# Performance work log

Hardware: AMD Instinct MI355X
Metric: run time of the kernel (lower is better)

Reference implementation:

```python
import jax, jax.numpy as jnp
import numpy as np

EPS = 1e-8
NEG_INF = -9e15  # matches torch masked_fill value


def setup_inputs() -> dict:
    key = jax.random.key(0)
    k1, k2 = jax.random.split(key)
    B, D = 4096, 512
    p1 = jax.random.normal(k1, (B, D), dtype=jnp.float32)
    p2 = jax.random.normal(k2, (B, D), dtype=jnp.float32)
    return {"p1": p1, "p2": p2}


def reference(p1, p2):
    # NT-Xent / InfoNCE loss as in SimCLR_MODEL.contrastive_loss (temperature = 1).
    z = jnp.concatenate([p1, p2], axis=0)              # [N, D], N = 2B
    # cosine similarity == GEMM of L2-normalized rows (torch eps clamp = 1e-8)
    zn = z / jnp.maximum(jnp.linalg.norm(z, axis=-1, keepdims=True), EPS)
    sim = zn @ zn.T                                     # [N, N]
    N = sim.shape[0]
    idx = jnp.arange(N)
    sim = sim.at[idx, idx].set(NEG_INF)                 # mask self-similarity
    # positive pair of row i is row (i + N/2) mod N (eye rolled by N/2)
    pos = sim[idx, (idx + N // 2) % N]                  # [N]
    nll = -pos + jax.nn.logsumexp(sim, axis=-1)
    return jnp.mean(nll)
```

## Files before the change

kernel.cpp:

```cpp
#include <hip/hip_runtime.h>
#include <hip/hip_bf16.h>
#include <math.h>

#define N_TOT 8192
#define HALF_N 4096
#define D_DIM 512
#define BM 256
#define BK 64
#define NKIT (D_DIM / BK)
#define NTILES 528
#define THREADS 512

#define WAIT_VM8 0xF78
#define WAIT_VM4 0xF74
#define WAIT_VM0 0xF70

typedef float f32x4_t __attribute__((ext_vector_type(4)));
typedef long long i64x2 __attribute__((ext_vector_type(2)));

typedef __attribute__((address_space(1))) unsigned int g_u32;
typedef __attribute__((address_space(3))) unsigned int l_u32;

__global__ __launch_bounds__(256) void k_normalize(
    const float* __restrict__ p1, const float* __restrict__ p2,
    unsigned char* __restrict__ zf8, float* __restrict__ rowsum,
    float* __restrict__ out)
{
    const int w = threadIdx.x >> 6;
    const int lane = threadIdx.x & 63;
    const int row = blockIdx.x * 4 + w;

    if (threadIdx.x < 4) rowsum[blockIdx.x * 4 + threadIdx.x] = 0.0f;
    if (blockIdx.x == 0 && threadIdx.x == 0) out[0] = 0.0f;

    const float* src = (row < HALF_N) ? p1 + (size_t)row * D_DIM
                                      : p2 + (size_t)(row - HALF_N) * D_DIM;
    float4 a = *(const float4*)(src + lane * 4);
    float4 b = *(const float4*)(src + 256 + lane * 4);
    float s = a.x*a.x + a.y*a.y + a.z*a.z + a.w*a.w
            + b.x*b.x + b.y*b.y + b.z*b.z + b.w*b.w;
    #pragma unroll
    for (int m = 1; m < 64; m <<= 1) s += __shfl_xor(s, m, 64);
    float inv = 1.0f / fmaxf(sqrtf(s), 1e-8f);

    int pk0 = __builtin_amdgcn_cvt_pk_fp8_f32(a.x * inv, a.y * inv, 0, false);
    pk0     = __builtin_amdgcn_cvt_pk_fp8_f32(a.z * inv, a.w * inv, pk0, true);
    int pk1 = __builtin_amdgcn_cvt_pk_fp8_f32(b.x * inv, b.y * inv, 0, false);
    pk1     = __builtin_amdgcn_cvt_pk_fp8_f32(b.z * inv, b.w * inv, pk1, true);

    unsigned char* dst = zf8 + (size_t)row * D_DIM;
    const int o0 = lane * 4;
    const int o1 = 256 + lane * 4;
    const int d0 = (o0 & ~63) + ((o0 >> 3) & 3) * 16 + ((o0 >> 5) & 1) * 8 + (o0 & 4);
    const int d1 = (o1 & ~63) + ((o1 >> 3) & 3) * 16 + ((o1 >> 5) & 1) * 8 + (o1 & 4);
    *(int*)(dst + d0) = pk0;
    *(int*)(dst + d1) = pk1;
}

__global__ __launch_bounds__(THREADS, 2) void k_gemm(
    const unsigned char* __restrict__ zf8,
    float* __restrict__ rowsum, float* __restrict__ pos)
{
    __shared__ __align__(16) unsigned char As[4][BM * BK];
    __shared__ __align__(16) unsigned char Bs[4][BM * BK];

    const int tid = threadIdx.x;
    const int lane = tid & 63;
    const int w = tid >> 6;
    const int wr = w >> 2, wc = w & 3;
    const int q = lane >> 4, l15 = lane & 15;

    const int t0 = blockIdx.x;
    const int t = (t0 & 7) * (NTILES / 8) + (t0 >> 3);

    int bi = (int)((sqrtf(8.0f * (float)t + 1.0f) - 1.0f) * 0.5f);
    while ((bi + 1) * (bi + 2) / 2 <= t) ++bi;
    while (bi * (bi + 1) / 2 > t) --bi;
    const int bx = bi;
    const int by = t - bi * (bi + 1) / 2;
    const bool isDiag = (bx == by);
    const bool hasPos = (bx - by == (HALF_N / BM));
    const int rowBase = by * BM;
    const int colBase = bx * BM;

    const int ci0 = tid;
    const int ci1 = tid + THREADS;
    const int r0 = ci0 >> 2, cc0 = ci0 & 3;
    const int r1 = ci1 >> 2, cc1 = ci1 & 3;
    const int gc0 = cc0 ^ ((r0 >> 1) & 3);
    const int gc1 = cc1 ^ ((r1 >> 1) & 3);

    const unsigned char* gA0 = zf8 + (size_t)(rowBase + r0) * D_DIM + gc0 * 16;
    const unsigned char* gA1 = zf8 + (size_t)(rowBase + r1) * D_DIM + gc1 * 16;
    const unsigned char* gB0 = zf8 + (size_t)(colBase + r0) * D_DIM + gc0 * 16;
    const unsigned char* gB1 = zf8 + (size_t)(colBase + r1) * D_DIM + gc1 * 16;

    auto stageAll = [&](int buf, int kblk) {
        const int kb = kblk * BK;
        __builtin_amdgcn_global_load_lds((const g_u32*)(gA0 + kb), (l_u32*)&As[buf][ci0 * 16], 16, 0, 0);
        __builtin_amdgcn_global_load_lds((const g_u32*)(gA1 + kb), (l_u32*)&As[buf][ci1 * 16], 16, 0, 0);
        __builtin_amdgcn_global_load_lds((const g_u32*)(gB0 + kb), (l_u32*)&Bs[buf][ci0 * 16], 16, 0, 0);
        __builtin_amdgcn_global_load_lds((const g_u32*)(gB1 + kb), (l_u32*)&Bs[buf][ci1 * 16], 16, 0, 0);
    };

    f32x4_t acc[8][4] = {};

#define READ_A(i) do { const int ra_ = wr * 128 + (i) * 16 + l15; \
        aF[i] = *(const i64x2*)&As[cur][ra_ * BK + (q ^ ((ra_ >> 1) & 3)) * 16]; } while (0)
#define READ_B(j) do { const int rb_ = wc * 64 + (j) * 16 + l15; \
        bF[j] = *(const i64x2*)&Bs[cur][rb_ * BK + (q ^ ((rb_ >> 1) & 3)) * 16]; } while (0)
#define QUAD(ih, jh) do { \
        __builtin_amdgcn_s_setprio(1); \
        _Pragma("unroll") for (int h_ = 0; h_ < 2; h_++) \
        _Pragma("unroll") for (int i_ = 0; i_ < 4; i_++) \
        _Pragma("unroll") for (int j_ = 0; j_ < 2; j_++) \
            acc[(ih) * 4 + i_][(jh) * 2 + j_] = __builtin_amdgcn_mfma_f32_16x16x32_fp8_fp8( \
                aF[(ih) * 4 + i_][h_], bF[(jh) * 2 + j_][h_], acc[(ih) * 4 + i_][(jh) * 2 + j_], 0, 0, 0); \
        __builtin_amdgcn_s_setprio(0); } while (0)

    stageAll(0, 0);
    stageAll(1, 1);
    stageAll(2, 2);
    __builtin_amdgcn_s_waitcnt(WAIT_VM8);
    __builtin_amdgcn_s_barrier();
    __builtin_amdgcn_sched_barrier(0);

    #pragma unroll
    for (int it = 0; it < NKIT; it++) {
        const int cur = it & 3;
        const int nslot = (it + 3) & 3;
        const bool doStage = (it + 3) < NKIT;
        const int kb = (it + 3) * BK;

        i64x2 aF[8], bF[4];

        READ_A(0); READ_A(1); READ_A(2); READ_A(3);
        READ_B(0); READ_B(1);
        if (doStage)
            __builtin_amdgcn_global_load_lds((const g_u32*)(gA0 + kb), (l_u32*)&As[nslot][ci0 * 16], 16, 0, 0);
        __builtin_amdgcn_s_barrier();
        QUAD(0, 0);
        __builtin_amdgcn_s_barrier();

        READ_B(2); READ_B(3);
        if (doStage)
            __builtin_amdgcn_global_load_lds((const g_u32*)(gA1 + kb), (l_u32*)&As[nslot][ci1 * 16], 16, 0, 0);
        __builtin_amdgcn_s_barrier();
        QUAD(0, 1);
        __builtin_amdgcn_s_barrier();

        READ_A(4); READ_A(5); READ_A(6); READ_A(7);
        if (doStage)
            __builtin_amdgcn_global_load_lds((const g_u32*)(gB0 + kb), (l_u32*)&Bs[nslot][ci0 * 16], 16, 0, 0);
        __builtin_amdgcn_s_barrier();
        QUAD(1, 0);
        __builtin_amdgcn_s_barrier();

        if (doStage)
            __builtin_amdgcn_global_load_lds((const g_u32*)(gB1 + kb), (l_u32*)&Bs[nslot][ci1 * 16], 16, 0, 0);
        __builtin_amdgcn_s_barrier();
        QUAD(1, 1);
        if (it < NKIT - 1) {
            if (it < 5)       __builtin_amdgcn_s_waitcnt(WAIT_VM8);
            else if (it == 5) __builtin_amdgcn_s_waitcnt(WAIT_VM4);
            else              __builtin_amdgcn_s_waitcnt(WAIT_VM0);
            __builtin_amdgcn_s_barrier();
            __builtin_amdgcn_sched_barrier(0);
        }
    }
#undef READ_A
#undef READ_B
#undef QUAD

    float colacc[4] = {0.f, 0.f, 0.f, 0.f};
    #pragma unroll
    for (int i = 0; i < 8; i++) {
        #pragma unroll
        for (int r = 0; r < 4; r++) {
            const int row = rowBase + wr * 128 + i * 16 + q * 4 + r;
            float rs = 0.0f;
            #pragma unroll
            for (int j = 0; j < 4; j++) {
                const int col = colBase + wc * 64 + j * 16 + l15;
                const float c = acc[i][j][r];
                float e = __expf(c);
                if (isDiag && col == row) e = 0.0f;
                rs += e;
                colacc[j] += e;
                if (hasPos && col == row + HALF_N) { pos[row] = c; pos[col] = c; }
            }
            rs += __shfl_xor(rs, 1); rs += __shfl_xor(rs, 2);
            rs += __shfl_xor(rs, 4); rs += __shfl_xor(rs, 8);
            if (l15 == 0) atomicAdd(&rowsum[row], rs);
        }
    }
    if (!isDiag) {
        #pragma unroll
        for (int j = 0; j < 4; j++) {
            float cs = colacc[j];
            cs += __shfl_xor(cs, 16);
            cs += __shfl_xor(cs, 32);
            if (q == 0) atomicAdd(&rowsum[colBase + wc * 64 + j * 16 + l15], cs);
        }
    }
}

__global__ __launch_bounds__(256) void k_finalize(
    const float* __restrict__ rowsum, const float* __restrict__ pos,
    float* __restrict__ out)
{
    const int t = threadIdx.x;
    const int i = blockIdx.x * 256 + t;
    float s = logf(rowsum[i]) - pos[i];
    #pragma unroll
    for (int m = 1; m < 64; m <<= 1) s += __shfl_xor(s, m, 64);
    __shared__ float red[4];
    if ((t & 63) == 0) red[t >> 6] = s;
    __syncthreads();
    if (t == 0)
        atomicAdd(out, (red[0] + red[1] + red[2] + red[3]) * (1.0f / (float)N_TOT));
}

extern "C" void kernel_launch(void* const* d_in, const int* in_sizes, int n_in,
                              void* d_out, int out_size, void* d_ws, size_t ws_size,
                              hipStream_t stream) {
    const float* p1 = (const float*)d_in[0];
    const float* p2 = (const float*)d_in[1];

    unsigned char* zf8 = (unsigned char*)d_ws;
    float* rowsum = (float*)((char*)d_ws + (size_t)N_TOT * D_DIM);
    float* pos    = rowsum + N_TOT;
    float* outp   = (float*)d_out;

    k_normalize<<<N_TOT / 4, 256, 0, stream>>>(p1, p2, zf8, rowsum, outp);
    k_gemm<<<NTILES, THREADS, 0, stream>>>(zf8, rowsum, pos);
    k_finalize<<<N_TOT / 256, 256, 0, stream>>>(rowsum, pos, outp);
}
```

Baseline: 123.3 us.

## Reduce GEMM LDS pipeline from four stages to double buffering

Shrinks the shared-memory staging for A and B tiles from four slots to two, prefetching only one K block ahead and waiting for all loads at each iteration end. This halves LDS use per block, which should let two blocks reside per CU and improve occupancy and tail balance across the 528 tiles. In exchange, the prefetch distance drops, so global-load latency is less hidden within a block. Scheduling barriers are also added after each staging barrier.

```diff
diff --git a/kernel.cpp b/kernel.cpp
--- a/kernel.cpp
+++ b/kernel.cpp
@@ -11,8 +11,6 @@
 #define NTILES 528
 #define THREADS 512
 
-#define WAIT_VM8 0xF78
-#define WAIT_VM4 0xF74
 #define WAIT_VM0 0xF70
 
 typedef float f32x4_t __attribute__((ext_vector_type(4)));
@@ -61,8 +59,8 @@
     const unsigned char* __restrict__ zf8,
     float* __restrict__ rowsum, float* __restrict__ pos)
 {
-    __shared__ __align__(16) unsigned char As[4][BM * BK];
-    __shared__ __align__(16) unsigned char Bs[4][BM * BK];
+    __shared__ __align__(16) unsigned char As[2][BM * BK];
+    __shared__ __align__(16) unsigned char Bs[2][BM * BK];
 
     const int tid = threadIdx.x;
     const int lane = tid & 63;
@@ -94,14 +92,6 @@
     const unsigned char* gA1 = zf8 + (size_t)(rowBase + r1) * D_DIM + gc1 * 16;
     const unsigned char* gB0 = zf8 + (size_t)(colBase + r0) * D_DIM + gc0 * 16;
     const unsigned char* gB1 = zf8 + (size_t)(colBase + r1) * D_DIM + gc1 * 16;
-
-    auto stageAll = [&](int buf, int kblk) {
-        const int kb = kblk * BK;
-        __builtin_amdgcn_global_load_lds((const g_u32*)(gA0 + kb), (l_u32*)&As[buf][ci0 * 16], 16, 0, 0);
-        __builtin_amdgcn_global_load_lds((const g_u32*)(gA1 + kb), (l_u32*)&As[buf][ci1 * 16], 16, 0, 0);
-        __builtin_amdgcn_global_load_lds((const g_u32*)(gB0 + kb), (l_u32*)&Bs[buf][ci0 * 16], 16, 0, 0);
-        __builtin_amdgcn_global_load_lds((const g_u32*)(gB1 + kb), (l_u32*)&Bs[buf][ci1 * 16], 16, 0, 0);
-    };
 
     f32x4_t acc[8][4] = {};
 
@@ -117,53 +107,55 @@
             acc[(ih) * 4 + i_][(jh) * 2 + j_] = __builtin_amdgcn_mfma_f32_16x16x32_fp8_fp8( \
                 aF[(ih) * 4 + i_][h_], bF[(jh) * 2 + j_][h_], acc[(ih) * 4 + i_][(jh) * 2 + j_], 0, 0, 0); \
         __builtin_amdgcn_s_setprio(0); } while (0)
-
-    stageAll(0, 0);
-    stageAll(1, 1);
-    stageAll(2, 2);
-    __builtin_amdgcn_s_waitcnt(WAIT_VM8);
+#define STAGE1(gp, arr, ci) \
+        __builtin_amdgcn_global_load_lds((const g_u32*)((gp) + kb), (l_u32*)&arr[nxt][(ci) * 16], 16, 0, 0)
+
+    {
+        const int nxt = 0; const int kb = 0;
+        STAGE1(gA0, As, ci0); STAGE1(gA1, As, ci1);
+        STAGE1(gB0, Bs, ci0); STAGE1(gB1, Bs, ci1);
+    }
+    __builtin_amdgcn_s_waitcnt(WAIT_VM0);
     __builtin_amdgcn_s_barrier();
     __builtin_amdgcn_sched_barrier(0);
 
     #pragma unroll
     for (int it = 0; it < NKIT; it++) {
-        const int cur = it & 3;
-        const int nslot = (it + 3) & 3;
-        const bool doStage = (it + 3) < NKIT;
-        const int kb = (it + 3) * BK;
+        const int cur = it & 1;
+        const int nxt = cur ^ 1;
+        const bool doStage = (it + 1 < NKIT);
+        const int kb = (it + 1) * BK;
 
         i64x2 aF[8], bF[4];
 
         READ_A(0); READ_A(1); READ_A(2); READ_A(3);
         READ_B(0); READ_B(1);
-        if (doStage)
-            __builtin_amdgcn_global_load_lds((const g_u32*)(gA0 + kb), (l_u32*)&As[nslot][ci0 * 16], 16, 0, 0);
-        __builtin_amdgcn_s_barrier();
+        if (doStage) STAGE1(gA0, As, ci0);
+        __builtin_amdgcn_s_barrier();
+        __builtin_amdgcn_sched_barrier(0);
         QUAD(0, 0);
         __builtin_amdgcn_s_barrier();
 
         READ_B(2); READ_B(3);
-        if (doStage)
-            __builtin_amdgcn_global_load_lds((const g_u32*)(gA1 + kb), (l_u32*)&As[nslot][ci1 * 16], 16, 0, 0);
-        __builtin_amdgcn_s_barrier();
+        if (doStage) STAGE1(gA1, As, ci1);
+        __builtin_amdgcn_s_barrier();
+        __builtin_amdgcn_sched_barrier(0);
         QUAD(0, 1);
         __builtin_amdgcn_s_barrier();
 
         READ_A(4); READ_A(5); READ_A(6); READ_A(7);
-        if (doStage)
-            __builtin_amdgcn_global_load_lds((const g_u32*)(gB0 + kb), (l_u32*)&Bs[nslot][ci0 * 16], 16, 0, 0);
-        __builtin_amdgcn_s_barrier();
+        if (doStage) STAGE1(gB0, Bs, ci0);
+        __builtin_amdgcn_s_barrier();
+        __builtin_amdgcn_sched_barrier(0);
         QUAD(1, 0);
         __builtin_amdgcn_s_barrier();
 
-        if (doStage)
-            __builtin_amdgcn_global_load_lds((const g_u32*)(gB1 + kb), (l_u32*)&Bs[nslot][ci1 * 16], 16, 0, 0);
-        __builtin_amdgcn_s_barrier();
+        if (doStage) STAGE1(gB1, Bs, ci1);
+        __builtin_amdgcn_s_barrier();
+        __builtin_amdgcn_sched_barrier(0);
         QUAD(1, 1);
-        if (it < NKIT - 1) {
-            if (it < 5)       __builtin_amdgcn_s_waitcnt(WAIT_VM8);
-            else if (it == 5) __builtin_amdgcn_s_waitcnt(WAIT_VM4);
-            else              __builtin_amdgcn_s_waitcnt(WAIT_VM0);
+        if (doStage) {
+            __builtin_amdgcn_s_waitcnt(WAIT_VM0);
             __builtin_amdgcn_s_barrier();
             __builtin_amdgcn_sched_barrier(0);
         }
@@ -171,6 +163,7 @@
 #undef READ_A
 #undef READ_B
 #undef QUAD
+#undef STAGE1
 
     float colacc[4] = {0.f, 0.f, 0.f, 0.f};
     #pragma unroll
```

Result: no change. 122.9 us (-0.3%).
